# Kernel optimization log

Hardware: AMD Instinct MI355X
Metric: run time of the kernel (lower is better)

The kernel has to match this reference:

```python
import jax, jax.numpy as jnp
import numpy as np

NUM_HEADS = 12

def setup_inputs() -> dict:
    key = jax.random.key(0)
    k1, k2 = jax.random.split(key)
    X = jax.random.normal(k1, (2, 2048, 768), dtype=jnp.float32)
    # torch nn.Linear(dim, 2*dim, bias=False) weight has shape [2*dim, dim]
    W_qkv = jax.random.normal(k2, (1536, 768), dtype=jnp.float32) * (768 ** -0.5)
    return {"X": X, "W_qkv": W_qkv}

def reference(X, W_qkv):
    B, N, C = X.shape
    H = NUM_HEADS
    hd = C // H
    scale = hd ** -0.5
    # qkv: [B, N, 2, H, hd]
    qkv = (X @ W_qkv.T).reshape(B, N, 2, H, hd)
    q = jnp.transpose(qkv[:, :, 0], (0, 2, 1, 3))  # [B, H, N, hd]
    k = jnp.transpose(qkv[:, :, 1], (0, 2, 1, 3))  # [B, H, N, hd]
    attn = jnp.einsum('bhnd,bhmd->bhnm', q, k) * scale  # [B, H, N, N]
    # dropout p=0 -> identity; double sum over heads and keys
    scores = attn.sum(axis=1).sum(axis=-1)  # [B, N]
    return scores
```

## Files before the change

kernel.cpp:

```cpp
#include <hip/hip_runtime.h>


#define DIM 768
#define SEQ 2048


__global__ void colsum_k(const float* __restrict__ X, float* __restrict__ xsum) {
    int b  = blockIdx.x >> 7;
    int ch = blockIdx.x & 127;
    int i  = threadIdx.x;
    const float4* base = (const float4*)(X + ((size_t)b * SEQ + (size_t)ch * 16) * DIM) + i;
    float4 a = {0.f, 0.f, 0.f, 0.f};
    #pragma unroll
    for (int n = 0; n < 16; ++n) {
        float4 x = base[n * 192];
        a.x += x.x; a.y += x.y; a.z += x.z; a.w += x.w;
    }
    float* dst = xsum + b * DIM + i * 4;
    atomicAdd(dst + 0, a.x);
    atomicAdd(dst + 1, a.y);
    atomicAdd(dst + 2, a.z);
    atomicAdd(dst + 3, a.w);
}

__global__ void vt_k(const float* __restrict__ W, const float* __restrict__ xsum,
                     float* __restrict__ t) {
    __shared__ float vv[4];
    int bi   = blockIdx.x;
    int b    = bi / 192;
    int c0   = (bi % 192) * 4;
    int tid  = threadIdx.x;
    int lane = tid & 63;
    int wv   = tid >> 6;

    {
        int c = c0 + wv;
        const float4* wr = (const float4*)(W + (size_t)(DIM + c) * DIM);
        const float4* xs = (const float4*)(xsum + b * DIM);
        float acc = 0.f;
        #pragma unroll
        for (int j = 0; j < 3; ++j) {
            float4 a = wr[lane + 64 * j];
            float4 s = xs[lane + 64 * j];
            acc += a.x * s.x + a.y * s.y + a.z * s.z + a.w * s.w;
        }
        #pragma unroll
        for (int off = 32; off; off >>= 1) acc += __shfl_down(acc, off, 64);
        if (lane == 0) vv[wv] = acc;
    }
    __syncthreads();

    float v0 = vv[0], v1 = vv[1], v2 = vv[2], v3 = vv[3];
    const float* w0 = W + (size_t)(c0 + 0) * DIM;
    const float* w1 = W + (size_t)(c0 + 1) * DIM;
    const float* w2 = W + (size_t)(c0 + 2) * DIM;
    const float* w3 = W + (size_t)(c0 + 3) * DIM;
    float* tb = t + b * DIM;
    #pragma unroll
    for (int k = 0; k < 3; ++k) {
        int d = tid + k * 256;
        float acc = v0 * w0[d] + v1 * w1[d] + v2 * w2[d] + v3 * w3[d];
        atomicAdd(&tb[d], acc);
    }
}

__global__ void scores_k(const float* __restrict__ X, const float* __restrict__ t,
                         float* __restrict__ out) {
    __shared__ alignas(16) float ft[DIM];
    int bi   = blockIdx.x;
    int b    = bi >> 8;
    int tid  = threadIdx.x;
    int lane = tid & 63;
    int wv   = tid >> 6;

    if (tid < 192)
        ((float4*)ft)[tid] = ((const float4*)(t + b * DIM))[tid];
    __syncthreads();

    const float4* t4 = (const float4*)ft;
    int r0 = bi * 8 + wv * 2;
    #pragma unroll
    for (int rr = 0; rr < 2; ++rr) {
        int r = r0 + rr;
        const float4* xr = (const float4*)(X + (size_t)r * DIM);
        float acc = 0.f;
        #pragma unroll
        for (int j = 0; j < 3; ++j) {
            float4 a = xr[lane + 64 * j];
            float4 s = t4[lane + 64 * j];
            acc += a.x * s.x + a.y * s.y + a.z * s.z + a.w * s.w;
        }
        #pragma unroll
        for (int off = 32; off; off >>= 1) acc += __shfl_down(acc, off, 64);
        if (lane == 0) out[r] = acc * 0.125f;
    }
}

extern "C" void kernel_launch(void* const* d_in, const int* in_sizes, int n_in,
                              void* d_out, int out_size, void* d_ws, size_t ws_size,
                              hipStream_t stream) {
    const float* X = (const float*)d_in[0];
    const float* W = (const float*)d_in[1];
    float* out = (float*)d_out;
    float* ws = (float*)d_ws;
    float* xsum = ws;
    float* t    = ws + 2 * DIM;

    colsum_k<<<256, 192, 0, stream>>>(X, xsum);
    vt_k    <<<384, 256, 0, stream>>>(W, xsum, t);
    scores_k<<<512, 256, 0, stream>>>(X, t, out);
}
```

Before: 87.76 us.

## Spread column-sum atomics over partial groups and coarsen weight-vector kernel blocks

The column-sum kernel now runs twice as many blocks with half the rows each and spreads its atomic adds across 16 partial-sum slots per batch, cutting contention on the same addresses. The second kernel first reduces those partials into shared memory, then each of 24 blocks handles 64 key channels instead of 4. This sharply reduces the number of atomic adds into t. The cost is far fewer blocks (24) on a large GPU, which may leave most compute units idle while W is streamed. The workspace must also be larger and zeroed for the partial slots.

```diff
diff --git a/kernel.cpp b/kernel.cpp
--- a/kernel.cpp
+++ b/kernel.cpp
@@ -3,63 +3,82 @@
 
 #define DIM 768
 #define SEQ 2048
+#define NGRP 16
 
 
-__global__ void colsum_k(const float* __restrict__ X, float* __restrict__ xsum) {
-    int b  = blockIdx.x >> 7;
-    int ch = blockIdx.x & 127;
+__global__ void colsum_k(const float* __restrict__ X, float* __restrict__ xpart) {
+    int bi = blockIdx.x;
+    int b  = bi >> 8;
+    int ch = bi & 255;
+    int g  = ch >> 4;
     int i  = threadIdx.x;
-    const float4* base = (const float4*)(X + ((size_t)b * SEQ + (size_t)ch * 16) * DIM) + i;
+    const float4* base = (const float4*)(X + ((size_t)b * SEQ + (size_t)ch * 8) * DIM) + i;
     float4 a = {0.f, 0.f, 0.f, 0.f};
     #pragma unroll
-    for (int n = 0; n < 16; ++n) {
+    for (int n = 0; n < 8; ++n) {
         float4 x = base[n * 192];
         a.x += x.x; a.y += x.y; a.z += x.z; a.w += x.w;
     }
-    float* dst = xsum + b * DIM + i * 4;
+    float* dst = xpart + ((size_t)(b * NGRP + g) * DIM) + i * 4;
     atomicAdd(dst + 0, a.x);
     atomicAdd(dst + 1, a.y);
     atomicAdd(dst + 2, a.z);
     atomicAdd(dst + 3, a.w);
 }
 
-__global__ void vt_k(const float* __restrict__ W, const float* __restrict__ xsum,
+__global__ void vt_k(const float* __restrict__ W, const float* __restrict__ xpart,
                      float* __restrict__ t) {
-    __shared__ float vv[4];
+    __shared__ alignas(16) float xs[DIM];
+    __shared__ float vv[64];
     int bi   = blockIdx.x;
-    int b    = bi / 192;
-    int c0   = (bi % 192) * 4;
+    int b    = bi / 12;
+    int c0   = (bi % 12) * 64;
     int tid  = threadIdx.x;
     int lane = tid & 63;
     int wv   = tid >> 6;
 
-    {
-        int c = c0 + wv;
-        const float4* wr = (const float4*)(W + (size_t)(DIM + c) * DIM);
-        const float4* xs = (const float4*)(xsum + b * DIM);
-        float acc = 0.f;
+    #pragma unroll
+    for (int k = 0; k < 3; ++k) {
+        int d = tid + k * 256;
+        const float* p = xpart + (size_t)(b * NGRP) * DIM + d;
+        float s = 0.f;
         #pragma unroll
-        for (int j = 0; j < 3; ++j) {
-            float4 a = wr[lane + 64 * j];
-            float4 s = xs[lane + 64 * j];
-            acc += a.x * s.x + a.y * s.y + a.z * s.z + a.w * s.w;
-        }
-        #pragma unroll
-        for (int off = 32; off; off >>= 1) acc += __shfl_down(acc, off, 64);
-        if (lane == 0) vv[wv] = acc;
+        for (int g = 0; g < NGRP; ++g)
+            s += p[(size_t)g * DIM];
+        xs[d] = s;
     }
     __syncthreads();
 
-    float v0 = vv[0], v1 = vv[1], v2 = vv[2], v3 = vv[3];
-    const float* w0 = W + (size_t)(c0 + 0) * DIM;
-    const float* w1 = W + (size_t)(c0 + 1) * DIM;
-    const float* w2 = W + (size_t)(c0 + 2) * DIM;
-    const float* w3 = W + (size_t)(c0 + 3) * DIM;
+    {
+        const float4* xs4 = (const float4*)xs;
+        float4 s0 = xs4[lane];
+        float4 s1 = xs4[lane + 64];
+        float4 s2 = xs4[lane + 128];
+        for (int i = 0; i < 16; ++i) {
+            int j = wv * 16 + i;
+            const float4* wr = (const float4*)(W + (size_t)(DIM + c0 + j) * DIM);
+            float4 a0 = wr[lane];
+            float4 a1 = wr[lane + 64];
+            float4 a2 = wr[lane + 128];
+            float acc = a0.x * s0.x + a0.y * s0.y + a0.z * s0.z + a0.w * s0.w
+                      + a1.x * s1.x + a1.y * s1.y + a1.z * s1.z + a1.w * s1.w
+                      + a2.x * s2.x + a2.y * s2.y + a2.z * s2.z + a2.w * s2.w;
+            #pragma unroll
+            for (int off = 32; off; off >>= 1) acc += __shfl_down(acc, off, 64);
+            if (lane == 0) vv[j] = acc;
+        }
+    }
+    __syncthreads();
+
     float* tb = t + b * DIM;
     #pragma unroll
     for (int k = 0; k < 3; ++k) {
         int d = tid + k * 256;
-        float acc = v0 * w0[d] + v1 * w1[d] + v2 * w2[d] + v3 * w3[d];
+        const float* wq = W + (size_t)c0 * DIM + d;
+        float acc = 0.f;
+        #pragma unroll 8
+        for (int j = 0; j < 64; ++j)
+            acc += vv[j] * wq[(size_t)j * DIM];
         atomicAdd(&tb[d], acc);
     }
 }
@@ -103,10 +122,10 @@
     const float* W = (const float*)d_in[1];
     float* out = (float*)d_out;
     float* ws = (float*)d_ws;
-    float* xsum = ws;
-    float* t    = ws + 2 * DIM;
+    float* xpart = ws;
+    float* t     = ws + 2 * NGRP * DIM;
 
-    colsum_k<<<256, 192, 0, stream>>>(X, xsum);
-    vt_k    <<<384, 256, 0, stream>>>(W, xsum, t);
+    colsum_k<<<512, 192, 0, stream>>>(X, xpart);
+    vt_k    <<<24, 256, 0, stream>>>(W, xpart, t);
     scores_k<<<512, 256, 0, stream>>>(X, t, out);
 }
```

Result: slower. 89.72 us (+2.2%).
